# Optimization experiments

Hardware: AMD Instinct MI355X
Metric: run time of the kernel (lower is better)

The kernel has to match this reference:

```python
import jax, jax.numpy as jnp
import numpy as np

D = 512
V = 32000
T = 2048
B = 4
R = 8          # n_rules
STEPS = 5      # ca_steps
GATE_SCALE = 0.001  # gate_mode='micro'
EPS = 1e-5


def _layer_norm(x, g, b):
    m = jnp.mean(x, axis=-1, keepdims=True)
    v = jnp.mean((x - m) ** 2, axis=-1, keepdims=True)
    return (x - m) * jax.lax.rsqrt(v + EPS) * g + b


def setup_inputs() -> dict:
    key = jax.random.key(0)
    ks = jax.random.split(key, 16)
    s_in = 1.0 / np.sqrt(3 * D)
    s_h = 1.0 / np.sqrt(2 * D)
    s_d = 1.0 / np.sqrt(D)
    return {
        "tokens": jax.random.randint(ks[0], (B, T), 0, V, dtype=jnp.int64),
        "gate_signal": jax.random.normal(ks[1], (1, T, D), dtype=jnp.float32),
        "embed": jax.random.normal(ks[2], (V, D), dtype=jnp.float32),
        "pos_embed": jax.random.normal(ks[3], (T, D), dtype=jnp.float32),
        "rule_w1": jax.random.normal(ks[4], (R, 3 * D, 2 * D), dtype=jnp.float32) * s_in,
        "rule_b1": jnp.zeros((R, 2 * D), dtype=jnp.float32),
        "rule_w2": jax.random.normal(ks[5], (R, 2 * D, D), dtype=jnp.float32) * s_h,
        "rule_b2": jnp.zeros((R, D), dtype=jnp.float32),
        "sel_w": jax.random.normal(ks[6], (D, R), dtype=jnp.float32) * s_d,
        "sel_b": jnp.zeros((R,), dtype=jnp.float32),
        "norm_g": jnp.ones((STEPS, D), dtype=jnp.float32),
        "norm_b": jnp.zeros((STEPS, D), dtype=jnp.float32),
        "lnf_g": jnp.ones((D,), dtype=jnp.float32),
        "lnf_b": jnp.zeros((D,), dtype=jnp.float32),
        "head_w": jax.random.normal(ks[7], (D, V), dtype=jnp.float32) * s_d,
    }


def reference(tokens, gate_signal, embed, pos_embed, rule_w1, rule_b1,
              rule_w2, rule_b2, sel_w, sel_b, norm_g, norm_b,
              lnf_g, lnf_b, head_w):
    # x = token embed + positional embed  -> [B,T,D]
    x = embed[tokens] + pos_embed[None, :, :]

    # rule selector: step-invariant in 'micro' mode -> [T,R]
    logits = (gate_signal[0] * GATE_SCALE) @ sel_w + sel_b
    rw = jax.nn.softmax(logits, axis=-1)  # [T,R]

    for step in range(STEPS):
        x_left = jnp.roll(x, 1, axis=1)   # cat([x[:,-1:], x[:,:-1]])
        x_right = jnp.roll(x, -1, axis=1)  # cat([x[:,1:], x[:,:1]])
        nb = jnp.concatenate([x, x_left, x_right], axis=-1)  # [B,T,3D]
        # all R rule MLPs batched
        h = jnp.einsum('btk,rkh->btrh', nb, rule_w1) + rule_b1  # [B,T,R,2D]
        h = jax.nn.gelu(h, approximate=False)
        ro = jnp.einsum('btrh,rhd->btrd', h, rule_w2) + rule_b2  # [B,T,R,D]
        evolved = jnp.einsum('btrd,tr->btd', ro, rw)
        x = _layer_norm(x + evolved, norm_g[step], norm_b[step])

    return _layer_norm(x, lnf_g, lnf_b) @ head_w  # [B,T,V]
```

## Files before the change

### kernel.cpp

```cpp
#include <hip/hip_runtime.h>

#define T_SEQ 2048
#define BT    8192
#define DM    512
#define NR    8
#define NSTEP 5
#define K1    1536
#define H2    1024
#define VSZ   32000
#define HN    8192

using ushort_t = unsigned short;
using bf16x8 = __attribute__((ext_vector_type(8))) __bf16;
using f32x4  = __attribute__((ext_vector_type(4))) float;

__device__ __forceinline__ ushort_t f2bf(float f) {
    union { float f; unsigned u; } v; v.f = f;
    unsigned r = v.u + 0x7FFFu + ((v.u >> 16) & 1u);
    return (ushort_t)(r >> 16);
}

__device__ __forceinline__ float bf2f(unsigned hi) {
    union { unsigned u; float f; } v; v.u = hi << 16;
    return v.f;
}

__device__ __forceinline__ void gload16(const void* g, void* l) {
    __builtin_amdgcn_global_load_lds((const __attribute__((address_space(1))) void*)g,
                                     (__attribute__((address_space(3))) void*)l, 16, 0, 0);
}

__device__ __forceinline__ float gelu_fast(float x) {
    float x2 = x * x;
    float u  = x * fmaf(x2, 0.10294456f, 2.3022861f);
    float e  = exp2f(-u);
    return x * __builtin_amdgcn_rcpf(1.0f + e);
}

#define BAR()    __builtin_amdgcn_s_barrier()
#define VMCNT4() asm volatile("s_waitcnt vmcnt(4)" ::: "memory")
#define VMCNT0() asm volatile("s_waitcnt vmcnt(0)" ::: "memory")

__global__ void transpose_f32_bf16(const float* __restrict__ src, ushort_t* __restrict__ dst,
                                   int K, int N, long long srcBatch, long long dstBatch, int dstRow)
{
    __shared__ float tile[32][33];
    src += (size_t)blockIdx.z * srcBatch;
    dst += (size_t)blockIdx.z * dstBatch;
    int n0 = blockIdx.x * 32, k0 = blockIdx.y * 32;
    int tx = threadIdx.x, ty = threadIdx.y;
    #pragma unroll
    for (int i = 0; i < 32; i += 8)
        tile[ty + i][tx] = src[(size_t)(k0 + ty + i) * N + (n0 + tx)];
    __syncthreads();
    #pragma unroll
    for (int i = 0; i < 32; i += 8)
        dst[(size_t)(n0 + ty + i) * dstRow + (k0 + tx)] = f2bf(tile[tx][ty + i]);
}

__global__ void embed_pos(const int* __restrict__ tokens, const float* __restrict__ emb,
                          const float* __restrict__ pos, float* __restrict__ x,
                          ushort_t* __restrict__ xbf)
{
    int row = blockIdx.x;
    int t = row & (T_SEQ - 1);
    int tok = tokens[row];
    int i = threadIdx.x;
    float2 e = ((const float2*)(emb + (size_t)tok * DM))[i];
    float2 p = ((const float2*)(pos + (size_t)t * DM))[i];
    float2 v = make_float2(e.x + p.x, e.y + p.y);
    ((float2*)(x + (size_t)row * DM))[i] = v;
    ushort_t bb[2] = { f2bf(v.x), f2bf(v.y) };
    ((unsigned*)(xbf + (size_t)row * DM))[i] = *(const unsigned*)bb;
}

__global__ void rw_kernel(const float* __restrict__ gate, const float* __restrict__ selw,
                          const float* __restrict__ selb, float* __restrict__ rw)
{
    int t = blockIdx.x, lane = threadIdx.x;
    float p[NR];
    #pragma unroll
    for (int r = 0; r < NR; ++r) p[r] = 0.f;
    for (int d = lane; d < DM; d += 64) {
        float gv = gate[(size_t)t * DM + d] * 0.001f;
        const float* swr = selw + (size_t)d * NR;
        #pragma unroll
        for (int r = 0; r < NR; ++r) p[r] += gv * swr[r];
    }
    #pragma unroll
    for (int o = 32; o; o >>= 1) {
        #pragma unroll
        for (int r = 0; r < NR; ++r) p[r] += __shfl_down(p[r], o, 64);
    }
    if (lane == 0) {
        float mx = -1e30f;
        #pragma unroll
        for (int r = 0; r < NR; ++r) { p[r] += selb[r]; mx = fmaxf(mx, p[r]); }
        float s = 0.f;
        #pragma unroll
        for (int r = 0; r < NR; ++r) { p[r] = expf(p[r] - mx); s += p[r]; }
        float inv = 1.0f / s;
        #pragma unroll
        for (int r = 0; r < NR; ++r) rw[t * NR + r] = p[r] * inv;
    }
}

template<int FINAL>
__global__ void ln_kernel(const float* __restrict__ xin, const ushort_t* __restrict__ evp,
                          const float* __restrict__ b2, const float* __restrict__ rwp,
                          const float* __restrict__ g, const float* __restrict__ b,
                          float* __restrict__ xout, ushort_t* __restrict__ xbf)
{
    __shared__ float sA[4], sB[4];
    int row = blockIdx.x, t = row & (T_SEQ - 1);
    int d = threadIdx.x << 1;
    float2 v = *(const float2*)(xin + (size_t)row * DM + d);
    float s0 = v.x, s1 = v.y;
    if (!FINAL) {
        #pragma unroll
        for (int sl = 0; sl < 4; ++sl) {
            unsigned u = ((const unsigned*)(evp + ((size_t)sl * BT + row) * DM))[threadIdx.x];
            s0 += bf2f(u & 0xffffu); s1 += bf2f(u >> 16);
        }
        #pragma unroll
        for (int r = 0; r < NR; ++r) {
            float w = rwp[t * NR + r];
            s0 += w * b2[r * DM + d];
            s1 += w * b2[r * DM + d + 1];
        }
    }
    float sum = s0 + s1, sq = s0 * s0 + s1 * s1;
    #pragma unroll
    for (int o = 32; o; o >>= 1) {
        sum += __shfl_down(sum, o, 64);
        sq  += __shfl_down(sq, o, 64);
    }
    int w = threadIdx.x >> 6;
    if ((threadIdx.x & 63) == 0) { sA[w] = sum; sB[w] = sq; }
    __syncthreads();
    sum = sA[0] + sA[1] + sA[2] + sA[3];
    sq  = sB[0] + sB[1] + sB[2] + sB[3];
    float mean = sum * (1.0f / DM);
    float var  = sq * (1.0f / DM) - mean * mean;
    float rstd = rsqrtf(var + 1e-5f);
    float o0 = (s0 - mean) * rstd * g[d] + b[d];
    float o1 = (s1 - mean) * rstd * g[d + 1] + b[d + 1];
    ushort_t bb[2] = { f2bf(o0), f2bf(o1) };
    ((unsigned*)(xbf + (size_t)row * DM))[threadIdx.x] = *(const unsigned*)bb;
    if (!FINAL)
        *(float2*)(xout + (size_t)row * DM + d) = make_float2(o0, o1);
}

template<int EPI, int AMODE, int FASTM>
__global__ __launch_bounds__(512, 2)
void gemm8(const ushort_t* __restrict__ A, const ushort_t* __restrict__ Bt,
           float* __restrict__ Cf, ushort_t* __restrict__ Cb,
           int nTileFast, int nPerSlice, int ktiles,
           int lda, int ldb, int ldc, long long sliceC,
           const float* __restrict__ bias, const float* __restrict__ rwp)
{
    __shared__ ushort_t As[2][256 * 64];
    __shared__ ushort_t Bs[2][256 * 64];

    const int tid  = threadIdx.x;
    const int wave = tid >> 6, lane = tid & 63;
    const int wm = wave >> 2, wn = wave & 3;

    int nwg = gridDim.x, bid = blockIdx.x;
    int qq = nwg >> 3, rr = nwg & 7, xc = bid & 7, wi = bid >> 3;
    int wgid = (xc < rr ? xc * (qq + 1) : rr * (qq + 1) + (xc - rr) * qq) + wi;
    int slice = wgid / nPerSlice, rem = wgid - slice * nPerSlice;
    int tA = rem / nTileFast, tB = rem - tA * nTileFast;
    int tm = FASTM ? tB : tA, tn = FASTM ? tA : tB;
    const int rowBase = tm * 256, colBase = tn * 256;
    const int kbase = slice * ktiles;
    if (EPI == 0) Cf += (long long)slice * sliceC;
    if (EPI == 2) Cb += (long long)slice * sliceC;

    const int lr  = lane >> 3;
    const int skE = (((lane & 7) ^ (lr & 7)) << 3);
    const ushort_t* Bsrc = Bt + (size_t)(colBase + wave * 32 + lr) * ldb + skE;
    const ushort_t* Asrc = A + (size_t)(rowBase + wave * 32 + lr) * lda + skE;

    auto stageA = [&](int t) {
        ushort_t* d = &As[t & 1][wave * 32 * 64];
        if (AMODE == 0) {
            const ushort_t* s = Asrc + (size_t)(kbase + t) * 64;
            #pragma unroll
            for (int j = 0; j < 4; ++j)
                gload16(s + (size_t)(j * 8) * lda, d + j * 512);
        } else {
            int seg  = t >> 3;
            int dts  = (seg == 0) ? 0 : (seg == 1 ? (T_SEQ - 1) : 1);
            int colE = ((t & 7) << 6) + skE;
            #pragma unroll
            for (int j = 0; j < 4; ++j) {
                int gr = rowBase + wave * 32 + j * 8 + lr;
                int sr = (gr & ~(T_SEQ - 1)) | ((gr + dts) & (T_SEQ - 1));
                gload16(A + (size_t)sr * DM + colE, d + j * 512);
            }
        }
    };
    auto stageB = [&](int t) {
        ushort_t* d = &Bs[t & 1][wave * 32 * 64];
        const ushort_t* s = Bsrc + (size_t)(kbase + t) * 64;
        #pragma unroll
        for (int j = 0; j < 4; ++j)
            gload16(s + (size_t)(j * 8) * ldb, d + j * 512);
    };

    const int l15 = lane & 15;
    const int sl0 = (((lane >> 4) ^ (lane & 7))) << 3;
    const int sl1 = (((lane >> 4) + 4) ^ (lane & 7)) << 3;
    const int aoff = (wm * 128 + l15) * 64;
    const int boff = (wn * 64 + l15) * 64;

    f32x4 acc[8][4] = {};
    bf16x8 Ar[2][2][4];
    bf16x8 Br[2][2][2];

    auto readAall = [&](int buf) {
        #pragma unroll
        for (int mh = 0; mh < 2; ++mh)
            #pragma unroll
            for (int m = 0; m < 4; ++m) {
                int base = aoff + mh * 4096 + m * 1024;
                Ar[mh][0][m] = *(const bf16x8*)&As[buf][base + sl0];
                Ar[mh][1][m] = *(const bf16x8*)&As[buf][base + sl1];
            }
    };
    auto readB = [&](int buf, int nh) {
        #pragma unroll
        for (int n = 0; n < 2; ++n) {
            int base = boff + nh * 2048 + n * 1024;
            Br[nh][0][n] = *(const bf16x8*)&Bs[buf][base + sl0];
            Br[nh][1][n] = *(const bf16x8*)&Bs[buf][base + sl1];
        }
    };
    auto mmaQ = [&](int mh, int nh) {
        #pragma unroll
        for (int k = 0; k < 2; ++k)
            #pragma unroll
            for (int m = 0; m < 4; ++m)
                #pragma unroll
                for (int n = 0; n < 2; ++n)
                    acc[mh * 4 + m][nh * 2 + n] = __builtin_amdgcn_mfma_f32_16x16x32_bf16(
                        Ar[mh][k][m], Br[nh][k][n], acc[mh * 4 + m][nh * 2 + n], 0, 0, 0);
    };

    stageA(0); stageB(0);
    if (ktiles > 1) stageA(1);
    VMCNT4();
    BAR();

    for (int t = 0; t < ktiles; ++t) {
        const int cur = t & 1;
        readAall(cur); readB(cur, 0);
        if (t + 1 < ktiles) stageB(t + 1);
        BAR();
        __builtin_amdgcn_s_setprio(1); mmaQ(0, 0); __builtin_amdgcn_s_setprio(0);
        BAR();
        readB(cur, 1);
        bool pre = (t + 2 < ktiles);
        if (pre) stageA(t + 2);
        BAR();
        __builtin_amdgcn_s_setprio(1); mmaQ(0, 1); __builtin_amdgcn_s_setprio(0);
        BAR();
        __builtin_amdgcn_s_setprio(1); mmaQ(1, 1); mmaQ(1, 0); __builtin_amdgcn_s_setprio(0);
        if (pre) { VMCNT4(); } else { VMCNT0(); }
        BAR();
    }

    const int cl = l15, rl = (lane >> 4) << 2;
    if constexpr (EPI == 0) {
        #pragma unroll
        for (int mf = 0; mf < 8; ++mf) {
            int gr = rowBase + wm * 128 + mf * 16 + rl;
            #pragma unroll
            for (int nf = 0; nf < 4; ++nf) {
                int gc = colBase + wn * 64 + nf * 16 + cl;
                #pragma unroll
                for (int i = 0; i < 4; ++i)
                    Cf[(size_t)(gr + i) * ldc + gc] = acc[mf][nf][i];
            }
        }
    } else if constexpr (EPI == 2) {
        #pragma unroll
        for (int mf = 0; mf < 8; ++mf) {
            int gr = rowBase + wm * 128 + mf * 16 + rl;
            #pragma unroll
            for (int nf = 0; nf < 4; ++nf) {
                int gc = colBase + wn * 64 + nf * 16 + cl;
                #pragma unroll
                for (int i = 0; i < 4; ++i)
                    Cb[(size_t)(gr + i) * ldc + gc] = f2bf(acc[mf][nf][i]);
            }
        }
    } else {
        int r = (colBase + wn * 64) >> 10;
        float bv[4];
        #pragma unroll
        for (int nf = 0; nf < 4; ++nf)
            bv[nf] = bias[r * H2 + ((colBase + wn * 64 + nf * 16 + cl) & (H2 - 1))];
        #pragma unroll
        for (int mf = 0; mf < 8; ++mf) {
            int gr = rowBase + wm * 128 + mf * 16 + rl;
            #pragma unroll
            for (int i = 0; i < 4; ++i) {
                float rwv = rwp[((gr + i) & (T_SEQ - 1)) * NR + r];
                #pragma unroll
                for (int nf = 0; nf < 4; ++nf) {
                    int gc = colBase + wn * 64 + nf * 16 + cl;
                    float v = acc[mf][nf][i] + bv[nf];
                    v = gelu_fast(v) * rwv;
                    Cb[(size_t)(gr + i) * ldc + gc] = f2bf(v);
                }
            }
        }
    }
}

extern "C" void kernel_launch(void* const* d_in, const int* in_sizes, int n_in,
                              void* d_out, int out_size, void* d_ws, size_t ws_size,
                              hipStream_t stream)
{
    const int*   tokens = (const int*)d_in[0];
    const float* gate   = (const float*)d_in[1];
    const float* emb    = (const float*)d_in[2];
    const float* pos    = (const float*)d_in[3];
    const float* w1     = (const float*)d_in[4];
    const float* b1     = (const float*)d_in[5];
    const float* w2     = (const float*)d_in[6];
    const float* b2     = (const float*)d_in[7];
    const float* selw   = (const float*)d_in[8];
    const float* selb   = (const float*)d_in[9];
    const float* ng     = (const float*)d_in[10];
    const float* nbm    = (const float*)d_in[11];
    const float* lnfg   = (const float*)d_in[12];
    const float* lnfb   = (const float*)d_in[13];
    const float* headw  = (const float*)d_in[14];
    float* out = (float*)d_out;
    (void)in_sizes; (void)n_in; (void)out_size; (void)ws_size;

    size_t off = 0;
    auto alloc = [&](size_t bytes) {
        void* p = (char*)d_ws + off;
        off += (bytes + 255) & ~(size_t)255;
        return p;
    };
    float*    x   = (float*)alloc((size_t)BT * DM * 4);
    ushort_t* xbf = (ushort_t*)alloc((size_t)BT * DM * 2);
    ushort_t* evp = (ushort_t*)alloc((size_t)4 * BT * DM * 2);
    ushort_t* W1t = (ushort_t*)alloc((size_t)NR * H2 * K1 * 2);
    ushort_t* W2t = (ushort_t*)alloc((size_t)DM * HN * 2);
    ushort_t* HWt = (ushort_t*)alloc((size_t)VSZ * DM * 2);
    float*    rw  = (float*)alloc((size_t)T_SEQ * NR * 4);
    ushort_t* H   = (ushort_t*)alloc((size_t)BT * HN * 2);

    transpose_f32_bf16<<<dim3(H2 / 32, K1 / 32, NR), dim3(32, 8), 0, stream>>>(
        w1, W1t, K1, H2, (long long)K1 * H2, (long long)H2 * K1, K1);
    transpose_f32_bf16<<<dim3(DM / 32, H2 / 32, NR), dim3(32, 8), 0, stream>>>(
        w2, W2t, H2, DM, (long long)H2 * DM, (long long)H2, HN);
    transpose_f32_bf16<<<dim3(VSZ / 32, DM / 32, 1), dim3(32, 8), 0, stream>>>(
        headw, HWt, DM, VSZ, 0LL, 0LL, DM);

    embed_pos<<<dim3(BT), dim3(256), 0, stream>>>(tokens, emb, pos, x, xbf);
    rw_kernel<<<dim3(T_SEQ), dim3(64), 0, stream>>>(gate, selw, selb, rw);

    for (int s = 0; s < NSTEP; ++s) {
        gemm8<1, 1, 1><<<dim3(1024), dim3(512), 0, stream>>>(
            xbf, W1t, nullptr, H, 32, 1024, K1 / 64,
            DM, K1, HN, 0LL, b1, rw);
        gemm8<2, 0, 0><<<dim3(256), dim3(512), 0, stream>>>(
            H, W2t, nullptr, evp, 2, 64, HN / 64 / 4,
            HN, HN, DM, (long long)BT * DM, nullptr, nullptr);
        ln_kernel<0><<<dim3(BT), dim3(256), 0, stream>>>(
            x, evp, b2, rw, ng + s * DM, nbm + s * DM, x, xbf);
    }

    ln_kernel<1><<<dim3(BT), dim3(256), 0, stream>>>(
        x, nullptr, nullptr, nullptr, lnfg, lnfb, nullptr, xbf);
    gemm8<0, 0, 0><<<dim3(4000), dim3(512), 0, stream>>>(
        xbf, HWt, out, nullptr, 125, 4000, DM / 64,
        DM, DM, VSZ, 0LL, nullptr, nullptr);
}
```

Measured before the change: 1.952 ms.

## Switch GEMMs to 32x32x16 MFMA with grouped tile rasterization

```diff
diff --git a/kernel.cpp b/kernel.cpp
--- a/kernel.cpp
+++ b/kernel.cpp
@@ -12,7 +12,7 @@
 
 using ushort_t = unsigned short;
 using bf16x8 = __attribute__((ext_vector_type(8))) __bf16;
-using f32x4  = __attribute__((ext_vector_type(4))) float;
+using f32x16 = __attribute__((ext_vector_type(16))) float;
 
 __device__ __forceinline__ ushort_t f2bf(float f) {
     union { float f; unsigned u; } v; v.f = f;
@@ -37,9 +37,10 @@
     return x * __builtin_amdgcn_rcpf(1.0f + e);
 }
 
-#define BAR()    __builtin_amdgcn_s_barrier()
-#define VMCNT4() asm volatile("s_waitcnt vmcnt(4)" ::: "memory")
-#define VMCNT0() asm volatile("s_waitcnt vmcnt(0)" ::: "memory")
+#define BAR()     __builtin_amdgcn_s_barrier()
+#define VMCNT4()  asm volatile("s_waitcnt vmcnt(4)" ::: "memory")
+#define VMCNT0()  asm volatile("s_waitcnt vmcnt(0)" ::: "memory")
+#define LGKM0()   asm volatile("s_waitcnt lgkmcnt(0)" ::: "memory")
 
 __global__ void transpose_f32_bf16(const float* __restrict__ src, ushort_t* __restrict__ dst,
                                    int K, int N, long long srcBatch, long long dstBatch, int dstRow)
@@ -151,13 +152,13 @@
         *(float2*)(xout + (size_t)row * DM + d) = make_float2(o0, o1);
 }
 
-template<int EPI, int AMODE, int FASTM>
+template<int EPI, int AMODE>
 __global__ __launch_bounds__(512, 2)
-void gemm8(const ushort_t* __restrict__ A, const ushort_t* __restrict__ Bt,
-           float* __restrict__ Cf, ushort_t* __restrict__ Cb,
-           int nTileFast, int nPerSlice, int ktiles,
-           int lda, int ldb, int ldc, long long sliceC,
-           const float* __restrict__ bias, const float* __restrict__ rwp)
+void gemm32(const ushort_t* __restrict__ A, const ushort_t* __restrict__ Bt,
+            float* __restrict__ Cf, ushort_t* __restrict__ Cb,
+            int nTmG, int nTnG, int gridTn, int nPerSlice, int ktiles, int nTnTot,
+            int lda, int ldb, int ldc, long long sliceC,
+            const float* __restrict__ bias, const float* __restrict__ rwp)
 {
     __shared__ ushort_t As[2][256 * 64];
     __shared__ ushort_t Bs[2][256 * 64];
@@ -170,8 +171,13 @@
     int qq = nwg >> 3, rr = nwg & 7, xc = bid & 7, wi = bid >> 3;
     int wgid = (xc < rr ? xc * (qq + 1) : rr * (qq + 1) + (xc - rr) * qq) + wi;
     int slice = wgid / nPerSlice, rem = wgid - slice * nPerSlice;
-    int tA = rem / nTileFast, tB = rem - tA * nTileFast;
-    int tm = FASTM ? tB : tA, tn = FASTM ? tA : tB;
+    int gsz = nTmG * nTnG;
+    int g = rem / gsz, li = rem - g * gsz;
+    int gTn = g % gridTn, gTm = g / gridTn;
+    int tm = gTm * nTmG + li / nTnG;
+    int tn = gTn * nTnG + li % nTnG;
+    if (tn >= nTnTot) return;
+
     const int rowBase = tm * 256, colBase = tn * 256;
     const int kbase = slice * ktiles;
     if (EPI == 0) Cf += (long long)slice * sliceC;
@@ -209,43 +215,37 @@
             gload16(s + (size_t)(j * 8) * ldb, d + j * 512);
     };
 
-    const int l15 = lane & 15;
-    const int sl0 = (((lane >> 4) ^ (lane & 7))) << 3;
-    const int sl1 = (((lane >> 4) + 4) ^ (lane & 7)) << 3;
-    const int aoff = (wm * 128 + l15) * 64;
-    const int boff = (wn * 64 + l15) * 64;
-
-    f32x4 acc[8][4] = {};
-    bf16x8 Ar[2][2][4];
-    bf16x8 Br[2][2][2];
-
-    auto readAall = [&](int buf) {
-        #pragma unroll
-        for (int mh = 0; mh < 2; ++mh)
-            #pragma unroll
-            for (int m = 0; m < 4; ++m) {
-                int base = aoff + mh * 4096 + m * 1024;
-                Ar[mh][0][m] = *(const bf16x8*)&As[buf][base + sl0];
-                Ar[mh][1][m] = *(const bf16x8*)&As[buf][base + sl1];
-            }
-    };
-    auto readB = [&](int buf, int nh) {
-        #pragma unroll
-        for (int n = 0; n < 2; ++n) {
-            int base = boff + nh * 2048 + n * 1024;
-            Br[nh][0][n] = *(const bf16x8*)&Bs[buf][base + sl0];
-            Br[nh][1][n] = *(const bf16x8*)&Bs[buf][base + sl1];
-        }
-    };
-    auto mmaQ = [&](int mh, int nh) {
-        #pragma unroll
-        for (int k = 0; k < 2; ++k)
-            #pragma unroll
-            for (int m = 0; m < 4; ++m)
-                #pragma unroll
-                for (int n = 0; n < 2; ++n)
-                    acc[mh * 4 + m][nh * 2 + n] = __builtin_amdgcn_mfma_f32_16x16x32_bf16(
-                        Ar[mh][k][m], Br[nh][k][n], acc[mh * 4 + m][nh * 2 + n], 0, 0, 0);
+    const int l31 = lane & 31, khalf = lane >> 5;
+    const int arow = wm * 128 + l31;
+    const int brow = wn * 64 + l31;
+
+    auto ldA = [&](int buf, int mf, int ks) -> bf16x8 {
+        int row = arow + mf * 32;
+        int slot = (ks * 2 + khalf) ^ (row & 7);
+        return *(const bf16x8*)&As[buf][row * 64 + slot * 8];
+    };
+    auto ldB = [&](int buf, int nf, int ks) -> bf16x8 {
+        int row = brow + nf * 32;
+        int slot = (ks * 2 + khalf) ^ (row & 7);
+        return *(const bf16x8*)&Bs[buf][row * 64 + slot * 8];
+    };
+
+    f32x16 acc[4][2] = {};
+    bf16x8 a0[4], a1[4], b0[2], b1[2];
+
+    auto mma2 = [&]() {
+        #pragma unroll
+        for (int mf = 0; mf < 4; ++mf)
+            #pragma unroll
+            for (int nf = 0; nf < 2; ++nf)
+                acc[mf][nf] = __builtin_amdgcn_mfma_f32_32x32x16_bf16(
+                    a0[mf], b0[nf], acc[mf][nf], 0, 0, 0);
+        #pragma unroll
+        for (int mf = 0; mf < 4; ++mf)
+            #pragma unroll
+            for (int nf = 0; nf < 2; ++nf)
+                acc[mf][nf] = __builtin_amdgcn_mfma_f32_32x32x16_bf16(
+                    a1[mf], b1[nf], acc[mf][nf], 0, 0, 0);
     };
 
     stageA(0); stageB(0);
@@ -255,68 +255,73 @@
 
     for (int t = 0; t < ktiles; ++t) {
         const int cur = t & 1;
-        readAall(cur); readB(cur, 0);
+        #pragma unroll
+        for (int mf = 0; mf < 4; ++mf) { a0[mf] = ldA(cur, mf, 0); a1[mf] = ldA(cur, mf, 1); }
+        #pragma unroll
+        for (int nf = 0; nf < 2; ++nf) { b0[nf] = ldB(cur, nf, 0); b1[nf] = ldB(cur, nf, 1); }
         if (t + 1 < ktiles) stageB(t + 1);
         BAR();
-        __builtin_amdgcn_s_setprio(1); mmaQ(0, 0); __builtin_amdgcn_s_setprio(0);
+        __builtin_amdgcn_s_setprio(1); mma2(); __builtin_amdgcn_s_setprio(0);
         BAR();
-        readB(cur, 1);
+        #pragma unroll
+        for (int mf = 0; mf < 4; ++mf) { a0[mf] = ldA(cur, mf, 2); a1[mf] = ldA(cur, mf, 3); }
+        #pragma unroll
+        for (int nf = 0; nf < 2; ++nf) { b0[nf] = ldB(cur, nf, 2); b1[nf] = ldB(cur, nf, 3); }
         bool pre = (t + 2 < ktiles);
-        if (pre) stageA(t + 2);
-        BAR();
-        __builtin_amdgcn_s_setprio(1); mmaQ(0, 1); __builtin_amdgcn_s_setprio(0);
-        BAR();
-        __builtin_amdgcn_s_setprio(1); mmaQ(1, 1); mmaQ(1, 0); __builtin_amdgcn_s_setprio(0);
+        if (pre) {
+            LGKM0();
+            BAR();
+            stageA(t + 2);
+        }
+        __builtin_amdgcn_s_setprio(1); mma2(); __builtin_amdgcn_s_setprio(0);
         if (pre) { VMCNT4(); } else { VMCNT0(); }
         BAR();
     }
 
-    const int cl = l15, rl = (lane >> 4) << 2;
     if constexpr (EPI == 0) {
         #pragma unroll
-        for (int mf = 0; mf < 8; ++mf) {
-            int gr = rowBase + wm * 128 + mf * 16 + rl;
-            #pragma unroll
-            for (int nf = 0; nf < 4; ++nf) {
-                int gc = colBase + wn * 64 + nf * 16 + cl;
+        for (int mf = 0; mf < 4; ++mf)
+            #pragma unroll
+            for (int nf = 0; nf < 2; ++nf) {
+                int gc = colBase + wn * 64 + nf * 32 + l31;
+                int rb = rowBase + wm * 128 + mf * 32 + 4 * khalf;
                 #pragma unroll
-                for (int i = 0; i < 4; ++i)
-                    Cf[(size_t)(gr + i) * ldc + gc] = acc[mf][nf][i];
-            }
-        }
-    } else if constexpr (EPI == 2) {
-        #pragma unroll
-        for (int mf = 0; mf < 8; ++mf) {
-            int gr = rowBase + wm * 128 + mf * 16 + rl;
-            #pragma unroll
-            for (int nf = 0; nf < 4; ++nf) {
-                int gc = colBase + wn * 64 + nf * 16 + cl;
-                #pragma unroll
-                for (int i = 0; i < 4; ++i)
-                    Cb[(size_t)(gr + i) * ldc + gc] = f2bf(acc[mf][nf][i]);
-            }
-        }
-    } else {
-        int r = (colBase + wn * 64) >> 10;
-        float bv[4];
-        #pragma unroll
-        for (int nf = 0; nf < 4; ++nf)
-            bv[nf] = bias[r * H2 + ((colBase + wn * 64 + nf * 16 + cl) & (H2 - 1))];
-        #pragma unroll
-        for (int mf = 0; mf < 8; ++mf) {
-            int gr = rowBase + wm * 128 + mf * 16 + rl;
-            #pragma unroll
-            for (int i = 0; i < 4; ++i) {
-                float rwv = rwp[((gr + i) & (T_SEQ - 1)) * NR + r];
-                #pragma unroll
-                for (int nf = 0; nf < 4; ++nf) {
-                    int gc = colBase + wn * 64 + nf * 16 + cl;
-                    float v = acc[mf][nf][i] + bv[nf];
-                    v = gelu_fast(v) * rwv;
-                    Cb[(size_t)(gr + i) * ldc + gc] = f2bf(v);
+                for (int r = 0; r < 16; ++r) {
+                    int grow = rb + (r & 3) + ((r >> 2) << 3);
+                    Cf[(size_t)grow * ldc + gc] = acc[mf][nf][r];
                 }
             }
-        }
+    } else if constexpr (EPI == 2) {
+        #pragma unroll
+        for (int mf = 0; mf < 4; ++mf)
+            #pragma unroll
+            for (int nf = 0; nf < 2; ++nf) {
+                int gc = colBase + wn * 64 + nf * 32 + l31;
+                int rb = rowBase + wm * 128 + mf * 32 + 4 * khalf;
+                #pragma unroll
+                for (int r = 0; r < 16; ++r) {
+                    int grow = rb + (r & 3) + ((r >> 2) << 3);
+                    Cb[(size_t)grow * ldc + gc] = f2bf(acc[mf][nf][r]);
+                }
+            }
+    } else {
+        #pragma unroll
+        for (int mf = 0; mf < 4; ++mf)
+            #pragma unroll
+            for (int nf = 0; nf < 2; ++nf) {
+                int cb = colBase + wn * 64 + nf * 32;
+                int gc = cb + l31;
+                int rule = cb >> 10;
+                float bv = bias[rule * H2 + (gc & (H2 - 1))];
+                int rb = rowBase + wm * 128 + mf * 32 + 4 * khalf;
+                #pragma unroll
+                for (int r = 0; r < 16; ++r) {
+                    int grow = rb + (r & 3) + ((r >> 2) << 3);
+                    float v = acc[mf][nf][r] + bv;
+                    v = gelu_fast(v) * rwp[(grow & (T_SEQ - 1)) * NR + rule];
+                    Cb[(size_t)grow * ldc + gc] = f2bf(v);
+                }
+            }
     }
 }
 
@@ -368,11 +373,11 @@
     rw_kernel<<<dim3(T_SEQ), dim3(64), 0, stream>>>(gate, selw, selb, rw);
 
     for (int s = 0; s < NSTEP; ++s) {
-        gemm8<1, 1, 1><<<dim3(1024), dim3(512), 0, stream>>>(
-            xbf, W1t, nullptr, H, 32, 1024, K1 / 64,
+        gemm32<1, 1><<<dim3(1024), dim3(512), 0, stream>>>(
+            xbf, W1t, nullptr, H, 8, 8, 4, 1024, K1 / 64, 32,
             DM, K1, HN, 0LL, b1, rw);
-        gemm8<2, 0, 0><<<dim3(256), dim3(512), 0, stream>>>(
-            H, W2t, nullptr, evp, 2, 64, HN / 64 / 4,
+        gemm32<2, 0><<<dim3(256), dim3(512), 0, stream>>>(
+            H, W2t, nullptr, evp, 8, 2, 1, 64, HN / 64 / 4, 2,
             HN, HN, DM, (long long)BT * DM, nullptr, nullptr);
         ln_kernel<0><<<dim3(BT), dim3(256), 0, stream>>>(
             x, evp, b2, rw, ng + s * DM, nbm + s * DM, x, xbf);
@@ -380,7 +385,7 @@
 
     ln_kernel<1><<<dim3(BT), dim3(256), 0, stream>>>(
         x, nullptr, nullptr, nullptr, lnfg, lnfb, nullptr, xbf);
-    gemm8<0, 0, 0><<<dim3(4000), dim3(512), 0, stream>>>(
-        xbf, HWt, out, nullptr, 125, 4000, DM / 64,
+    gemm32<0, 0><<<dim3(4096), dim3(512), 0, stream>>>(
+        xbf, HWt, out, nullptr, 8, 8, 16, 4096, DM / 64, 125,
         DM, DM, VSZ, 0LL, nullptr, nullptr);
 }
```

Result: slower. 2.123 ms (+8.8%).

## Fuse final LayerNorm into last step, precompute bias mix, group-swizzle GEMM tiles

Applied to the files above, without the earlier changes.

```diff
diff --git a/kernel.cpp b/kernel.cpp
--- a/kernel.cpp
+++ b/kernel.cpp
@@ -75,7 +75,8 @@
 }
 
 __global__ void rw_kernel(const float* __restrict__ gate, const float* __restrict__ selw,
-                          const float* __restrict__ selb, float* __restrict__ rw)
+                          const float* __restrict__ selb, const float* __restrict__ b2,
+                          float* __restrict__ rw, float* __restrict__ b2rw)
 {
     int t = blockIdx.x, lane = threadIdx.x;
     float p[NR];
@@ -90,72 +91,107 @@
     #pragma unroll
     for (int o = 32; o; o >>= 1) {
         #pragma unroll
-        for (int r = 0; r < NR; ++r) p[r] += __shfl_down(p[r], o, 64);
-    }
-    if (lane == 0) {
-        float mx = -1e30f;
-        #pragma unroll
-        for (int r = 0; r < NR; ++r) { p[r] += selb[r]; mx = fmaxf(mx, p[r]); }
-        float s = 0.f;
-        #pragma unroll
-        for (int r = 0; r < NR; ++r) { p[r] = expf(p[r] - mx); s += p[r]; }
-        float inv = 1.0f / s;
-        #pragma unroll
-        for (int r = 0; r < NR; ++r) rw[t * NR + r] = p[r] * inv;
-    }
-}
-
-template<int FINAL>
-__global__ void ln_kernel(const float* __restrict__ xin, const ushort_t* __restrict__ evp,
-                          const float* __restrict__ b2, const float* __restrict__ rwp,
-                          const float* __restrict__ g, const float* __restrict__ b,
-                          float* __restrict__ xout, ushort_t* __restrict__ xbf)
-{
-    __shared__ float sA[4], sB[4];
-    int row = blockIdx.x, t = row & (T_SEQ - 1);
-    int d = threadIdx.x << 1;
-    float2 v = *(const float2*)(xin + (size_t)row * DM + d);
-    float s0 = v.x, s1 = v.y;
-    if (!FINAL) {
-        #pragma unroll
-        for (int sl = 0; sl < 4; ++sl) {
-            unsigned u = ((const unsigned*)(evp + ((size_t)sl * BT + row) * DM))[threadIdx.x];
-            s0 += bf2f(u & 0xffffu); s1 += bf2f(u >> 16);
-        }
-        #pragma unroll
-        for (int r = 0; r < NR; ++r) {
-            float w = rwp[t * NR + r];
-            s0 += w * b2[r * DM + d];
-            s1 += w * b2[r * DM + d + 1];
-        }
-    }
-    float sum = s0 + s1, sq = s0 * s0 + s1 * s1;
-    #pragma unroll
-    for (int o = 32; o; o >>= 1) {
-        sum += __shfl_down(sum, o, 64);
-        sq  += __shfl_down(sq, o, 64);
-    }
-    int w = threadIdx.x >> 6;
-    if ((threadIdx.x & 63) == 0) { sA[w] = sum; sB[w] = sq; }
-    __syncthreads();
-    sum = sA[0] + sA[1] + sA[2] + sA[3];
-    sq  = sB[0] + sB[1] + sB[2] + sB[3];
+        for (int r = 0; r < NR; ++r) p[r] += __shfl_xor(p[r], o, 64);
+    }
+    float mx = -1e30f;
+    #pragma unroll
+    for (int r = 0; r < NR; ++r) { p[r] += selb[r]; mx = fmaxf(mx, p[r]); }
+    float s = 0.f;
+    #pragma unroll
+    for (int r = 0; r < NR; ++r) { p[r] = expf(p[r] - mx); s += p[r]; }
+    float inv = 1.0f / s;
+    #pragma unroll
+    for (int r = 0; r < NR; ++r) p[r] *= inv;
+    if (lane < NR) rw[t * NR + lane] = p[lane];
+    #pragma unroll
+    for (int it = 0; it < DM / 64; ++it) {
+        int d = it * 64 + lane;
+        float a = 0.f;
+        #pragma unroll
+        for (int r = 0; r < NR; ++r) a += p[r] * b2[r * DM + d];
+        b2rw[(size_t)t * DM + d] = a;
+    }
+}
+
+template<int MODE>
+__global__ __launch_bounds__(256)
+void ln_kernel(const float* __restrict__ xin, const ushort_t* __restrict__ evp,
+               const float* __restrict__ b2rw,
+               const float* __restrict__ g, const float* __restrict__ b,
+               const float* __restrict__ fg, const float* __restrict__ fb,
+               float* __restrict__ xout, ushort_t* __restrict__ xbf)
+{
+    int row = (blockIdx.x << 2) + (threadIdx.x >> 6);
+    int lane = threadIdx.x & 63;
+    int t = row & (T_SEQ - 1);
+    int d0 = lane << 3;
+
+    float s[8];
+    {
+        float4 a = *(const float4*)(xin + (size_t)row * DM + d0);
+        float4 c = *(const float4*)(xin + (size_t)row * DM + d0 + 4);
+        s[0]=a.x; s[1]=a.y; s[2]=a.z; s[3]=a.w; s[4]=c.x; s[5]=c.y; s[6]=c.z; s[7]=c.w;
+    }
+    #pragma unroll
+    for (int sl = 0; sl < 4; ++sl) {
+        uint4 u = *(const uint4*)(evp + ((size_t)sl * BT + row) * DM + d0);
+        const unsigned w[4] = { u.x, u.y, u.z, u.w };
+        #pragma unroll
+        for (int j = 0; j < 4; ++j) {
+            s[2*j]   += bf2f(w[j] & 0xffffu);
+            s[2*j+1] += bf2f(w[j] >> 16);
+        }
+    }
+    {
+        float4 a = *(const float4*)(b2rw + (size_t)t * DM + d0);
+        float4 c = *(const float4*)(b2rw + (size_t)t * DM + d0 + 4);
+        s[0]+=a.x; s[1]+=a.y; s[2]+=a.z; s[3]+=a.w; s[4]+=c.x; s[5]+=c.y; s[6]+=c.z; s[7]+=c.w;
+    }
+    float sum = 0.f, sq = 0.f;
+    #pragma unroll
+    for (int j = 0; j < 8; ++j) { sum += s[j]; sq += s[j] * s[j]; }
+    #pragma unroll
+    for (int o = 32; o; o >>= 1) { sum += __shfl_xor(sum, o, 64); sq += __shfl_xor(sq, o, 64); }
     float mean = sum * (1.0f / DM);
     float var  = sq * (1.0f / DM) - mean * mean;
     float rstd = rsqrtf(var + 1e-5f);
-    float o0 = (s0 - mean) * rstd * g[d] + b[d];
-    float o1 = (s1 - mean) * rstd * g[d + 1] + b[d + 1];
-    ushort_t bb[2] = { f2bf(o0), f2bf(o1) };
-    ((unsigned*)(xbf + (size_t)row * DM))[threadIdx.x] = *(const unsigned*)bb;
-    if (!FINAL)
-        *(float2*)(xout + (size_t)row * DM + d) = make_float2(o0, o1);
-}
-
-template<int EPI, int AMODE, int FASTM>
+
+    float o8[8];
+    #pragma unroll
+    for (int j = 0; j < 8; ++j)
+        o8[j] = (s[j] - mean) * rstd * g[d0 + j] + b[d0 + j];
+
+    if constexpr (MODE == 0) {
+        float4 w0 = make_float4(o8[0], o8[1], o8[2], o8[3]);
+        float4 w1 = make_float4(o8[4], o8[5], o8[6], o8[7]);
+        *(float4*)(xout + (size_t)row * DM + d0) = w0;
+        *(float4*)(xout + (size_t)row * DM + d0 + 4) = w1;
+        ushort_t bb[8];
+        #pragma unroll
+        for (int j = 0; j < 8; ++j) bb[j] = f2bf(o8[j]);
+        *(uint4*)(xbf + (size_t)row * DM + d0) = *(const uint4*)bb;
+    } else {
+        float sum2 = 0.f, sq2 = 0.f;
+        #pragma unroll
+        for (int j = 0; j < 8; ++j) { sum2 += o8[j]; sq2 += o8[j] * o8[j]; }
+        #pragma unroll
+        for (int o = 32; o; o >>= 1) { sum2 += __shfl_xor(sum2, o, 64); sq2 += __shfl_xor(sq2, o, 64); }
+        float m2 = sum2 * (1.0f / DM);
+        float v2 = sq2 * (1.0f / DM) - m2 * m2;
+        float r2 = rsqrtf(v2 + 1e-5f);
+        ushort_t bb[8];
+        #pragma unroll
+        for (int j = 0; j < 8; ++j)
+            bb[j] = f2bf((o8[j] - m2) * r2 * fg[d0 + j] + fb[d0 + j]);
+        *(uint4*)(xbf + (size_t)row * DM + d0) = *(const uint4*)bb;
+    }
+}
+
+template<int EPI, int AMODE>
 __global__ __launch_bounds__(512, 2)
 void gemm8(const ushort_t* __restrict__ A, const ushort_t* __restrict__ Bt,
            float* __restrict__ Cf, ushort_t* __restrict__ Cb,
-           int nTileFast, int nPerSlice, int ktiles,
+           int nTmG, int nTnG, int gridTn, int nPerSlice, int ktiles, int nTnTot,
            int lda, int ldb, int ldc, long long sliceC,
            const float* __restrict__ bias, const float* __restrict__ rwp)
 {
@@ -170,8 +206,13 @@
     int qq = nwg >> 3, rr = nwg & 7, xc = bid & 7, wi = bid >> 3;
     int wgid = (xc < rr ? xc * (qq + 1) : rr * (qq + 1) + (xc - rr) * qq) + wi;
     int slice = wgid / nPerSlice, rem = wgid - slice * nPerSlice;
-    int tA = rem / nTileFast, tB = rem - tA * nTileFast;
-    int tm = FASTM ? tB : tA, tn = FASTM ? tA : tB;
+    int gsz = nTmG * nTnG;
+    int g = rem / gsz, li = rem - g * gsz;
+    int gTn = g % gridTn, gTm = g / gridTn;
+    int tm = gTm * nTmG + li / nTnG;
+    int tn = gTn * nTnG + li % nTnG;
+    if (tn >= nTnTot) return;
+
     const int rowBase = tm * 256, colBase = tn * 256;
     const int kbase = slice * ktiles;
     if (EPI == 0) Cf += (long long)slice * sliceC;
@@ -348,14 +389,15 @@
         off += (bytes + 255) & ~(size_t)255;
         return p;
     };
-    float*    x   = (float*)alloc((size_t)BT * DM * 4);
-    ushort_t* xbf = (ushort_t*)alloc((size_t)BT * DM * 2);
-    ushort_t* evp = (ushort_t*)alloc((size_t)4 * BT * DM * 2);
-    ushort_t* W1t = (ushort_t*)alloc((size_t)NR * H2 * K1 * 2);
-    ushort_t* W2t = (ushort_t*)alloc((size_t)DM * HN * 2);
-    ushort_t* HWt = (ushort_t*)alloc((size_t)VSZ * DM * 2);
-    float*    rw  = (float*)alloc((size_t)T_SEQ * NR * 4);
-    ushort_t* H   = (ushort_t*)alloc((size_t)BT * HN * 2);
+    float*    x    = (float*)alloc((size_t)BT * DM * 4);
+    ushort_t* xbf  = (ushort_t*)alloc((size_t)BT * DM * 2);
+    ushort_t* evp  = (ushort_t*)alloc((size_t)4 * BT * DM * 2);
+    ushort_t* W1t  = (ushort_t*)alloc((size_t)NR * H2 * K1 * 2);
+    ushort_t* W2t  = (ushort_t*)alloc((size_t)DM * HN * 2);
+    ushort_t* HWt  = (ushort_t*)alloc((size_t)VSZ * DM * 2);
+    float*    rw   = (float*)alloc((size_t)T_SEQ * NR * 4);
+    float*    b2rw = (float*)alloc((size_t)T_SEQ * DM * 4);
+    ushort_t* H    = (ushort_t*)alloc((size_t)BT * HN * 2);
 
     transpose_f32_bf16<<<dim3(H2 / 32, K1 / 32, NR), dim3(32, 8), 0, stream>>>(
         w1, W1t, K1, H2, (long long)K1 * H2, (long long)H2 * K1, K1);
@@ -365,22 +407,28 @@
         headw, HWt, DM, VSZ, 0LL, 0LL, DM);
 
     embed_pos<<<dim3(BT), dim3(256), 0, stream>>>(tokens, emb, pos, x, xbf);
-    rw_kernel<<<dim3(T_SEQ), dim3(64), 0, stream>>>(gate, selw, selb, rw);
+    rw_kernel<<<dim3(T_SEQ), dim3(64), 0, stream>>>(gate, selw, selb, b2, rw, b2rw);
 
     for (int s = 0; s < NSTEP; ++s) {
-        gemm8<1, 1, 1><<<dim3(1024), dim3(512), 0, stream>>>(
-            xbf, W1t, nullptr, H, 32, 1024, K1 / 64,
+        gemm8<1, 1><<<dim3(1024), dim3(512), 0, stream>>>(
+            xbf, W1t, nullptr, H, 32, 1, 32,
+            1024, K1 / 64, 32,
             DM, K1, HN, 0LL, b1, rw);
-        gemm8<2, 0, 0><<<dim3(256), dim3(512), 0, stream>>>(
-            H, W2t, nullptr, evp, 2, 64, HN / 64 / 4,
+        gemm8<2, 0><<<dim3(256), dim3(512), 0, stream>>>(
+            H, W2t, nullptr, evp, 32, 2, 1,
+            64, HN / 64 / 4, 2,
             HN, HN, DM, (long long)BT * DM, nullptr, nullptr);
-        ln_kernel<0><<<dim3(BT), dim3(256), 0, stream>>>(
-            x, evp, b2, rw, ng + s * DM, nbm + s * DM, x, xbf);
-    }
-
-    ln_kernel<1><<<dim3(BT), dim3(256), 0, stream>>>(
-        x, nullptr, nullptr, nullptr, lnfg, lnfb, nullptr, xbf);
-    gemm8<0, 0, 0><<<dim3(4000), dim3(512), 0, stream>>>(
-        xbf, HWt, out, nullptr, 125, 4000, DM / 64,
+        if (s < NSTEP - 1) {
+            ln_kernel<0><<<dim3(BT / 4), dim3(256), 0, stream>>>(
+                x, evp, b2rw, ng + s * DM, nbm + s * DM, nullptr, nullptr, x, xbf);
+        } else {
+            ln_kernel<2><<<dim3(BT / 4), dim3(256), 0, stream>>>(
+                x, evp, b2rw, ng + s * DM, nbm + s * DM, lnfg, lnfb, nullptr, xbf);
+        }
+    }
+
+    gemm8<0, 0><<<dim3(4096), dim3(512), 0, stream>>>(
+        xbf, HWt, out, nullptr, 8, 4, 32,
+        4096, DM / 64, 125,
         DM, DM, VSZ, 0LL, nullptr, nullptr);
 }
```

New measurement: 1.948 ms. No clear change (-0.2%).
